# Optimization experiments

Hardware: AMD Instinct MI355X
Metric: run time of the kernel (lower is better)

Reference implementation:

```python
import jax, jax.numpy as jnp
import numpy as np

B, L = 2, 4096
EMBED_DIM, NUM_HEADS, WINDOW = 1024, 16, 256
NUM_EXPERTS, TOP_K, FF_HIDDEN = 8, 2, 4096
ENTROPY_W, MAX_USAGE = 0.1, 0.3


def setup_inputs() -> dict:
    key = jax.random.key(0)
    ks = jax.random.split(key, 10)
    s = 0.02
    C, F, E = EMBED_DIM, FF_HIDDEN, NUM_EXPERTS
    return {
        "x": jax.random.normal(ks[0], (B, L, C), jnp.float32),
        "g1": jnp.ones((C,), jnp.float32), "b1": jnp.zeros((C,), jnp.float32),
        "g2": jnp.ones((C,), jnp.float32), "b2": jnp.zeros((C,), jnp.float32),
        "g3": jnp.ones((C,), jnp.float32), "b3": jnp.zeros((C,), jnp.float32),
        "Wqkv": jax.random.normal(ks[1], (C, 3 * C), jnp.float32) * s, "bqkv": jnp.zeros((3 * C,), jnp.float32),
        "Wo": jax.random.normal(ks[2], (C, C), jnp.float32) * s, "bo": jnp.zeros((C,), jnp.float32),
        "conv_w": jax.random.normal(ks[3], (C, C, 3), jnp.float32) * s, "conv_b": jnp.zeros((C,), jnp.float32),
        "gate_W": jax.random.normal(ks[4], (C, E), jnp.float32) * s, "gate_b": jnp.zeros((E,), jnp.float32),
        "expert_W": jax.random.normal(ks[5], (E, C, C), jnp.float32) * s, "expert_b": jnp.zeros((E, C), jnp.float32),
        "ff_W1": jax.random.normal(ks[6], (C, F), jnp.float32) * s, "ff_b1": jnp.zeros((F,), jnp.float32),
        "ff_W2": jax.random.normal(ks[7], (F, C), jnp.float32) * s, "ff_b2": jnp.zeros((C,), jnp.float32),
    }


def _ln(x, g, b):
    mu = x.mean(-1, keepdims=True)
    var = ((x - mu) ** 2).mean(-1, keepdims=True)
    return (x - mu) * jax.lax.rsqrt(var + 1e-5) * g + b


def _local_attn(x, Wqkv, bqkv, Wo, bo):
    # Faithful port of the unfold-based overlapping-window attention
    Bsz, Ln, C = x.shape
    hd = C // NUM_HEADS
    pad = (-Ln) % WINDOW
    xp = jnp.pad(x, ((0, 0), (0, pad), (0, 0)))
    Lp = Ln + pad
    qkv = (xp @ Wqkv + bqkv).reshape(Bsz, Lp, 3, NUM_HEADS, hd).transpose(2, 0, 3, 1, 4)
    q, k, v = qkv[0], qkv[1], qkv[2]  # [B,H,Lp,hd]
    step = WINDOW // 2  # bidirectional=True -> overlapping windows
    nw = (Lp - WINDOW) // step + 1
    idx = (jnp.arange(nw) * step)[:, None] + jnp.arange(WINDOW)[None, :]  # [nw,w]

    def win(t):
        # torch unfold(dim=2,size=w,step) puts window on LAST axis -> [B,H,nw,hd,w]
        return jnp.swapaxes(t[:, :, idx, :], -1, -2)

    qw, kw, vw = win(q), win(k), win(v)
    # q @ k^T over the window axis (exactly what the torch code computes)
    attn = jax.nn.softmax(jnp.einsum('bhnds,bhnes->bhnde', qw, kw) * hd ** -0.5, axis=-1)
    o = jnp.einsum('bhnde,bhnes->bhnds', attn, vw)  # [B,H,nw,hd,w]
    o = o.reshape(Bsz, NUM_HEADS, nw * WINDOW, hd).transpose(0, 2, 1, 3).reshape(Bsz, nw * WINDOW, C)
    return (o @ Wo + bo)[:, :Ln]


def _dconv(x, w, b):
    # Conv1d(C,C,k=3,dilation=2,padding='same'); w is [O,I,K]
    y = jax.lax.conv_general_dilated(jnp.swapaxes(x, 1, 2), w, (1,), 'SAME',
                                     rhs_dilation=(2,), dimension_numbers=('NCH', 'OIH', 'NCH'))
    return jnp.swapaxes(y + b[None, :, None], 1, 2)


def _moe(x, gW, gb, eW, eb):
    Bsz, S, C = x.shape
    N = Bsz * S
    xf = x.reshape(N, C)
    probs = jax.nn.softmax(xf @ gW + gb, axis=-1)
    entropy = -jnp.sum(probs * jnp.log(probs + 1e-10), axis=-1).mean()
    topk_p, topk_i = jax.lax.top_k(probs, TOP_K)  # [N,K]
    # dense-equivalent top-k dispatch: out[n] = sum_k p_k * expert_{i_k}(x_n)
    eo = jnp.einsum('nc,ech->neh', xf, eW) + eb  # [N,E,C]
    combine = jnp.zeros((N, NUM_EXPERTS), xf.dtype).at[jnp.arange(N)[:, None], topk_i].add(topk_p)
    out = jnp.einsum('neh,ne->nh', eo, combine)
    counts = jnp.zeros((NUM_EXPERTS,), jnp.float32).at[topk_i.reshape(-1)].add(1.0)
    penalty = jnp.sum(jax.nn.relu(counts / N - MAX_USAGE))
    return out.reshape(Bsz, S, C), ENTROPY_W * entropy + penalty


def reference(x, g1, b1, g2, b2, g3, b3, Wqkv, bqkv, Wo, bo, conv_w, conv_b,
              gate_W, gate_b, expert_W, expert_b, ff_W1, ff_b1, ff_W2, ff_b2):
    x = x + _local_attn(_ln(x, g1, b1), Wqkv, bqkv, Wo, bo)
    x = x + _dconv(_ln(x, g2, b2), conv_w, conv_b)
    moe_out, aux = _moe(_ln(x, g3, b3), gate_W, gate_b, expert_W, expert_b)
    x = x + moe_out
    x = x + (jax.nn.gelu(x @ ff_W1 + ff_b1, approximate=False) @ ff_W2 + ff_b2)
    return x, aux
```

## Files before the change

### kernel.cpp

```cpp
#include <hip/hip_runtime.h>
#include <cmath>

typedef _Float16 f16;
typedef __attribute__((ext_vector_type(8))) _Float16 f16x8;
typedef __attribute__((ext_vector_type(4))) _Float16 f16x4;
typedef __attribute__((ext_vector_type(4))) float f32x4;

struct TileInfo { int m0, mcnt, e, pad; };

__device__ __forceinline__ void gload16(const void* g, void* l) {
  __builtin_amdgcn_global_load_lds((const __attribute__((address_space(1))) void*)g,
                                   (__attribute__((address_space(3))) void*)l, 16, 0, 0);
}

__device__ __forceinline__ float fast_gelu(float u) {
  const float c = u * (0.7978845608028654f + 0.0356774081f * u * u);
  const float t = fminf(2.0f * c, 80.0f);
  const float e = __expf(t);
  return u * (e * __builtin_amdgcn_rcpf(e + 1.0f));
}

template<int NPASS, int MODE, int EPI>
__global__ __launch_bounds__(256)
void gemm_kernel(const f16* __restrict__ Ah, const f16* __restrict__ Al, int lda,
                 const f16* __restrict__ Bh, const f16* __restrict__ Bl, int ldb,
                 const float* __restrict__ bias, const float* __restrict__ res,
                 float* __restrict__ outf, f16* __restrict__ outh, int ldo, int K,
                 const int* __restrict__ rowmap, const TileInfo* __restrict__ table,
                 const char* __restrict__ zbuf) {
  __shared__ __align__(16) char lds[65536];

  const int tid  = threadIdx.x;
  const int wave = tid >> 6;
  const int lane = tid & 63;

  int m0, mcnt, eidx = 0;
  if (MODE == 2) {
    TileInfo ti = table[blockIdx.x];
    if (ti.mcnt <= 0) return;
    m0 = ti.m0; mcnt = ti.mcnt; eidx = ti.e;
  } else { m0 = blockIdx.x * 128; mcnt = 128; }
  const int n0 = blockIdx.y * 128;

  const f16* Bh_ = Bh;
  const float* bias_ = bias;
  size_t adelta = 0, bdelta = 0;
  if (NPASS == 3) {
    adelta = (size_t)((const char*)Al - (const char*)Ah);
    bdelta = (size_t)((const char*)Bl - (const char*)Bh);
  }
  if (MODE == 2) { Bh_ += ((size_t)eidx << 20); bias_ += eidx * 1024; }

  f32x4 acc[4][4] = {};
  const int wm  = (wave >> 1) * 64;
  const int wn  = (wave & 1) * 64;
  const int fr  = lane & 15;
  const int kgb = (lane >> 4) * 16;
  const int wuni = wave * 1024;

  if constexpr (NPASS == 1) {
    const int sr    = tid / 8;
    const int cbyte = (tid % 8) * 16;
    const char* aSrc[4];
    const char* bSrc[4];
    #pragma unroll
    for (int r = 0; r < 4; ++r) {
      const int mr  = sr + r * 32;
      const int cbs = cbyte ^ ((mr & 7) << 4);
      int gi = m0 + ((mr < mcnt) ? mr : (mcnt - 1));
      if (MODE == 1 || MODE == 2) gi = rowmap[gi];
      aSrc[r] = (const char*)Ah + (size_t)gi * lda * 2 + cbs;
      const int nr   = sr + r * 32;
      const int ncbs = cbyte ^ ((nr & 7) << 4);
      bSrc[r] = (const char*)Bh_ + (size_t)(n0 + nr) * ldb * 2 + ncbs;
    }
    const int NT = K / 64;
    #pragma unroll
    for (int r = 0; r < 4; ++r) {
      gload16(aSrc[r], lds + r * 4096 + wuni);
      gload16(bSrc[r], lds + 16384 + r * 4096 + wuni);
    }
    #pragma unroll
    for (int r = 0; r < 4; ++r) {
      gload16(aSrc[r] + 128, lds + 32768 + r * 4096 + wuni);
      gload16(bSrc[r] + 128, lds + 32768 + 16384 + r * 4096 + wuni);
    }
    asm volatile("s_waitcnt vmcnt(8)" ::: "memory");
    __builtin_amdgcn_s_barrier();

    for (int kt = 0; kt < NT; ++kt) {
      const int c = kt & 1;
      const char* LAp = lds + c * 32768;
      const char* LBp = LAp + 16384;
      f16x8 ah[2][4], bh[2][4];
      #pragma unroll
      for (int kk = 0; kk < 2; ++kk) {
        #pragma unroll
        for (int i = 0; i < 4; ++i) {
          const int ar = wm + i * 16 + fr;
          ah[kk][i] = *(const f16x8*)(LAp + ar * 128 + ((kk * 64 + kgb) ^ ((ar & 7) << 4)));
          const int br = wn + i * 16 + fr;
          bh[kk][i] = *(const f16x8*)(LBp + br * 128 + ((kk * 64 + kgb) ^ ((br & 7) << 4)));
        }
      }
      asm volatile("s_waitcnt lgkmcnt(0)" ::: "memory");
      __builtin_amdgcn_s_barrier();
      if (kt + 2 < NT) {
        const size_t ko = (size_t)(kt + 2) * 128;
        #pragma unroll
        for (int r = 0; r < 4; ++r) {
          gload16(aSrc[r] + ko, lds + c * 32768 + r * 4096 + wuni);
          gload16(bSrc[r] + ko, lds + c * 32768 + 16384 + r * 4096 + wuni);
        }
      }
      #pragma unroll
      for (int kk = 0; kk < 2; ++kk)
        #pragma unroll
        for (int i = 0; i < 4; ++i)
          #pragma unroll
          for (int j = 0; j < 4; ++j)
            acc[i][j] = __builtin_amdgcn_mfma_f32_16x16x32_f16(ah[kk][i], bh[kk][j], acc[i][j], 0, 0, 0);
      if (kt + 2 < NT) asm volatile("s_waitcnt vmcnt(8)" ::: "memory");
      else             asm volatile("s_waitcnt vmcnt(0)" ::: "memory");
      __builtin_amdgcn_s_barrier();
    }
  } else {
    const int sr3 = tid >> 2;
    const int cb3 = (tid & 3) * 16;
    int aRow3[2], aCbs3[2], aOff3[2], bOff3[2];
    #pragma unroll
    for (int q = 0; q < 2; ++q) {
      const int row = q * 64 + sr3;
      const int cbs = cb3 ^ (((row >> 1) & 3) << 4);
      int gi = m0 + row;
      if (MODE == 1) gi = rowmap[m0 + row];
      aRow3[q] = gi; aCbs3[q] = cbs;
      aOff3[q] = gi * lda * 2 + cbs;
      bOff3[q] = (n0 + row) * ldb * 2 + cbs;
    }
    const int NT = K / 32;

    auto STAGE3 = [&](int kt2, char* bb) {
      const int k0 = kt2 * 32;
      #pragma unroll
      for (int q = 0; q < 2; ++q) {
        const char* as; const char* asl;
        if (MODE == 3) {
          const int tap = k0 >> 10;
          const int kc  = k0 & 1023;
          const int tok = aRow3[q] & 4095;
          const int st  = tok + (tap - 1) * 2;
          if (st >= 0 && st < 4096) {
            as  = (const char*)Ah + (size_t)(aRow3[q] + (tap - 1) * 2) * 2048 + kc * 2 + aCbs3[q];
            asl = as + adelta;
          } else { as = zbuf; asl = zbuf; }
        } else {
          as  = (const char*)Ah + (size_t)aOff3[q] + (size_t)k0 * 2;
          asl = as + adelta;
        }
        gload16(as,  bb + q * 4096 + wuni);
        gload16(asl, bb + 8192 + q * 4096 + wuni);
        const char* bs = (const char*)Bh_ + (size_t)bOff3[q] + (size_t)k0 * 2;
        gload16(bs,          bb + 16384 + q * 4096 + wuni);
        gload16(bs + bdelta, bb + 24576 + q * 4096 + wuni);
      }
    };

    STAGE3(0, lds);
    STAGE3(1, lds + 32768);
    asm volatile("s_waitcnt vmcnt(8)" ::: "memory");
    __builtin_amdgcn_s_barrier();

    for (int kt = 0; kt < NT; ++kt) {
      char* bb = lds + (kt & 1) * 32768;
      f16x8 ah[4], al[4], bh[4], bl[4];
      #pragma unroll
      for (int i = 0; i < 4; ++i) {
        const int ar = wm + i * 16 + fr;
        const int ao = ar * 64 + (kgb ^ (((ar >> 1) & 3) << 4));
        ah[i] = *(const f16x8*)(bb + ao);
        al[i] = *(const f16x8*)(bb + 8192 + ao);
        const int br = wn + i * 16 + fr;
        const int bo = br * 64 + (kgb ^ (((br >> 1) & 3) << 4));
        bh[i] = *(const f16x8*)(bb + 16384 + bo);
        bl[i] = *(const f16x8*)(bb + 24576 + bo);
      }
      asm volatile("s_waitcnt lgkmcnt(0)" ::: "memory");
      __builtin_amdgcn_s_barrier();
      if (kt + 2 < NT) STAGE3(kt + 2, bb);
      #pragma unroll
      for (int i = 0; i < 4; ++i)
        #pragma unroll
        for (int j = 0; j < 4; ++j) {
          acc[i][j] = __builtin_amdgcn_mfma_f32_16x16x32_f16(ah[i], bh[j], acc[i][j], 0, 0, 0);
          acc[i][j] = __builtin_amdgcn_mfma_f32_16x16x32_f16(ah[i], bl[j], acc[i][j], 0, 0, 0);
          acc[i][j] = __builtin_amdgcn_mfma_f32_16x16x32_f16(al[i], bh[j], acc[i][j], 0, 0, 0);
        }
      if (kt + 2 < NT) asm volatile("s_waitcnt vmcnt(8)" ::: "memory");
      else             asm volatile("s_waitcnt vmcnt(0)" ::: "memory");
      __builtin_amdgcn_s_barrier();
    }
  }

  #pragma unroll
  for (int i = 0; i < 4; ++i) {
    const int mb = wm + i * 16 + (lane >> 4) * 4;
    #pragma unroll
    for (int j = 0; j < 4; ++j) {
      const int nc = n0 + wn + j * 16 + fr;
      const float bv = bias_[nc];
      #pragma unroll
      for (int q = 0; q < 4; ++q) {
        const int ml = mb + q;
        if (MODE == 2 && ml >= mcnt) continue;
        const size_t orow = (size_t)(m0 + ml);
        float v = acc[i][j][q] + bv;
        if (EPI == 1) v += res[orow * ldo + nc];
        if (EPI == 3) v = fast_gelu(v);
        if (EPI <= 1) outf[orow * ldo + nc] = v;
        else          outh[orow * ldo + nc] = (f16)v;
      }
    }
  }
}

template<int WLO, int WGATE>
__global__ __launch_bounds__(256)
void ln_kernel(const float* __restrict__ x, const float* __restrict__ g, const float* __restrict__ b,
               f16* __restrict__ oh, f16* __restrict__ ol,
               const float* __restrict__ gW, const float* __restrict__ gb,
               float* __restrict__ logits) {
  const int row = blockIdx.x;
  const int t = threadIdx.x;
  const float4 v = ((const float4*)(x + (size_t)row * 1024))[t];
  float s  = v.x + v.y + v.z + v.w;
  float ss = v.x * v.x + v.y * v.y + v.z * v.z + v.w * v.w;
  #pragma unroll
  for (int off = 32; off; off >>= 1) { s += __shfl_down(s, off, 64); ss += __shfl_down(ss, off, 64); }
  __shared__ float red[8];
  if ((t & 63) == 0) { red[t >> 6] = s; red[(t >> 6) + 4] = ss; }
  __syncthreads();
  s  = red[0] + red[1] + red[2] + red[3];
  ss = red[4] + red[5] + red[6] + red[7];
  const float mu  = s * (1.0f / 1024.0f);
  const float var = ss * (1.0f / 1024.0f) - mu * mu;
  const float inv = 1.0f / sqrtf(var + 1e-5f);
  const float4 gv = ((const float4*)g)[t];
  const float4 bv = ((const float4*)b)[t];
  float y[4];
  y[0] = (v.x - mu) * inv * gv.x + bv.x;
  y[1] = (v.y - mu) * inv * gv.y + bv.y;
  y[2] = (v.z - mu) * inv * gv.z + bv.z;
  y[3] = (v.w - mu) * inv * gv.w + bv.w;
  f16x4 hv;
  #pragma unroll
  for (int u = 0; u < 4; ++u) hv[u] = (f16)y[u];
  *(f16x4*)(oh + (size_t)row * 1024 + t * 4) = hv;
  if (WLO) {
    f16x4 lv;
    #pragma unroll
    for (int u = 0; u < 4; ++u) lv[u] = (f16)(y[u] - (float)hv[u]);
    *(f16x4*)(ol + (size_t)row * 1024 + t * 4) = lv;
  }
  if (WGATE) {
    const float* gr = gW + (size_t)(t * 4) * 8;
    float lg[8];
    #pragma unroll
    for (int e = 0; e < 8; ++e)
      lg[e] = y[0] * gr[e] + y[1] * gr[8 + e] + y[2] * gr[16 + e] + y[3] * gr[24 + e];
    #pragma unroll
    for (int m = 1; m < 64; m <<= 1)
      #pragma unroll
      for (int e = 0; e < 8; ++e) lg[e] += __shfl_xor(lg[e], m, 64);
    __shared__ float gred[4][8];
    if ((t & 63) == 0) {
      #pragma unroll
      for (int e = 0; e < 8; ++e) gred[t >> 6][e] = lg[e];
    }
    __syncthreads();
    if (t < 8)
      logits[(size_t)row * 8 + t] = gred[0][t] + gred[1][t] + gred[2][t] + gred[3][t] + gb[t];
  }
}

__global__ __launch_bounds__(512, 4)
void attn_kernel(const float* __restrict__ qkv, f16* __restrict__ oh, f16* __restrict__ ol) {
  __shared__ __align__(16) char sm[81920];
  const int bid = blockIdx.x;
  const int b = bid >> 8, h = (bid >> 4) & 15, n = bid & 15;
  const int t = threadIdx.x;
  const size_t rowbase = (size_t)(b * 2176 + n * 128);
  const char* qg = (const char*)(qkv + rowbase * 3072 + h * 64);
  const char* kg = qg + 4096;
  const char* vg = qg + 8192;

  const int srow = t >> 4;
  const int scol = (t & 15) * 16;
  const int wuni = (t >> 6) * 1024;

  const int dt = t >> 4;
  const int et = t & 15;
  float pacc[2][4] = {};

  for (int r = 0; r < 2; ++r) {
    #pragma unroll
    for (int p = 0; p < 4; ++p) {
      const size_t off = (size_t)(r * 128 + p * 32 + srow) * 12288 + scol;
      gload16(qg + off, sm + p * 8192 + wuni);
      gload16(kg + off, sm + 32768 + p * 8192 + wuni);
    }
    __syncthreads();
    #pragma unroll 4
    for (int s = 0; s < 128; ++s) {
      const float2 q2 = *(const float2*)(sm + s * 256 + dt * 8);
      const f32x4 k4 = *(const f32x4*)(sm + 32768 + s * 256 + et * 16);
      #pragma unroll
      for (int z = 0; z < 4; ++z) {
        pacc[0][z] += q2.x * k4[z];
        pacc[1][z] += q2.y * k4[z];
      }
    }
    __syncthreads();
  }

  #pragma unroll
  for (int i = 0; i < 2; ++i) {
    #pragma unroll
    for (int z = 0; z < 4; ++z) pacc[i][z] *= 0.125f;
    float m = fmaxf(fmaxf(pacc[i][0], pacc[i][1]), fmaxf(pacc[i][2], pacc[i][3]));
    m = fmaxf(m, __shfl_xor(m, 1, 16));
    m = fmaxf(m, __shfl_xor(m, 2, 16));
    m = fmaxf(m, __shfl_xor(m, 4, 16));
    m = fmaxf(m, __shfl_xor(m, 8, 16));
    float den = 0.0f;
    #pragma unroll
    for (int z = 0; z < 4; ++z) { pacc[i][z] = __expf(pacc[i][z] - m); den += pacc[i][z]; }
    den += __shfl_xor(den, 1, 16);
    den += __shfl_xor(den, 2, 16);
    den += __shfl_xor(den, 4, 16);
    den += __shfl_xor(den, 8, 16);
    const float dinv = 1.0f / den;
    f32x4 pv;
    #pragma unroll
    for (int z = 0; z < 4; ++z) pv[z] = pacc[i][z] * dinv;
    *(f32x4*)(sm + 65536 + (dt * 2 + i) * 256 + et * 16) = pv;
  }

  const int dt2 = t & 15;
  const int st  = t >> 4;
  const int ch  = h * 64 + (st & 15) * 4;
  const size_t rb2 = (size_t)(b * 4096 + n * 256);

  for (int c = 0; c < 2; ++c) {
    __syncthreads();
    #pragma unroll
    for (int p = 0; p < 4; ++p) {
      const size_t off = (size_t)(c * 128 + p * 32 + srow) * 12288 + scol;
      gload16(vg + off, sm + p * 8192 + wuni);
    }
    __syncthreads();
    float o[16];
    #pragma unroll
    for (int u = 0; u < 16; ++u) o[u] = 0.0f;
    #pragma unroll 2
    for (int e4 = 0; e4 < 16; ++e4) {
      f32x4 p4[4], v4[4];
      #pragma unroll
      for (int i = 0; i < 4; ++i)
        p4[i] = *(const f32x4*)(sm + 65536 + (dt2 * 4 + i) * 256 + e4 * 16);
      #pragma unroll
      for (int j = 0; j < 4; ++j)
        v4[j] = *(const f32x4*)(sm + (st * 4 + j) * 256 + e4 * 16);
      #pragma unroll
      for (int j = 0; j < 4; ++j)
        #pragma unroll
        for (int i = 0; i < 4; ++i) {
          o[j * 4 + i] += v4[j][0] * p4[i][0] + v4[j][1] * p4[i][1]
                        + v4[j][2] * p4[i][2] + v4[j][3] * p4[i][3];
        }
    }
    const int rq = c * 2 + (st >> 4);
    #pragma unroll
    for (int i = 0; i < 4; ++i) {
      const size_t row = rb2 + (size_t)(dt2 * 4 + i) * 4 + rq;
      f16x4 hv, lv;
      #pragma unroll
      for (int j = 0; j < 4; ++j) {
        const float val = o[j * 4 + i];
        hv[j] = (f16)val;
        lv[j] = (f16)(val - (float)hv[j]);
      }
      *(f16x4*)(oh + row * 1024 + ch) = hv;
      *(f16x4*)(ol + row * 1024 + ch) = lv;
    }
  }
}

template<int SPLIT>
__global__ __launch_bounds__(256)
void transpose_kernel(const float* __restrict__ in, int R, int Cc,
                      f16* __restrict__ oh, f16* __restrict__ ol) {
  __shared__ float tile[32][33];
  const size_t mat = (size_t)blockIdx.z * R * Cc;
  in += mat; oh += mat; if (SPLIT) ol += mat;
  const int tx = threadIdx.x & 31, ty = threadIdx.x >> 5;
  const int c = blockIdx.x * 32 + tx;
  #pragma unroll
  for (int j = 0; j < 32; j += 8) {
    const int r = blockIdx.y * 32 + ty + j;
    tile[ty + j][tx] = in[(size_t)r * Cc + c];
  }
  __syncthreads();
  const int rT = blockIdx.y * 32 + tx;
  #pragma unroll
  for (int j = 0; j < 32; j += 8) {
    const int cT = blockIdx.x * 32 + ty + j;
    const float v = tile[tx][ty + j];
    const f16 hv = (f16)v;
    oh[(size_t)cT * R + rT] = hv;
    if (SPLIT) ol[(size_t)cT * R + rT] = (f16)(v - (float)hv);
  }
}

__global__ __launch_bounds__(256)
void convw_kernel(const float* __restrict__ w, f16* __restrict__ oh, f16* __restrict__ ol) {
  const int id = blockIdx.x * 256 + threadIdx.x;
  const int o = id >> 10, i = id & 1023;
  const float* ws = w + (size_t)o * 3072 + i * 3;
  #pragma unroll
  for (int tap = 0; tap < 3; ++tap) {
    const float v = ws[tap];
    const f16 hv = (f16)v;
    const size_t oi = (size_t)o * 3072 + tap * 1024 + i;
    oh[oi] = hv;
    ol[oi] = (f16)(v - (float)hv);
  }
}

__global__ void qkvrows_kernel(int* __restrict__ rows) {
  const int r = blockIdx.x * 256 + threadIdx.x;
  if (r < 4352) rows[r] = (r >= 2176) ? (4096 + r - 2176) : r;
}

__global__ __launch_bounds__(256)
void gatefin_kernel(const float* __restrict__ logits, float* __restrict__ top2p,
                    int* __restrict__ top2i, float* __restrict__ ent,
                    int* __restrict__ counts) {
  __shared__ int hist[8];
  const int t = threadIdx.x;
  if (t < 8) hist[t] = 0;
  __syncthreads();
  const int token = blockIdx.x * 256 + t;
  float lg[8];
  const float4 l0 = ((const float4*)(logits + (size_t)token * 8))[0];
  const float4 l1 = ((const float4*)(logits + (size_t)token * 8))[1];
  lg[0] = l0.x; lg[1] = l0.y; lg[2] = l0.z; lg[3] = l0.w;
  lg[4] = l1.x; lg[5] = l1.y; lg[6] = l1.z; lg[7] = l1.w;
  int i0 = 0; float v0 = lg[0];
  #pragma unroll
  for (int e = 1; e < 8; ++e) if (lg[e] > v0) { v0 = lg[e]; i0 = e; }
  int i1 = 0; float v1 = -1e30f;
  #pragma unroll
  for (int e = 0; e < 8; ++e) if (e != i0 && lg[e] > v1) { v1 = lg[e]; i1 = e; }
  float den = 0.0f; float pr[8];
  #pragma unroll
  for (int e = 0; e < 8; ++e) { pr[e] = __expf(lg[e] - v0); den += pr[e]; }
  const float dinv = 1.0f / den;
  float H = 0.0f, p0 = 0.0f, p1 = 0.0f;
  #pragma unroll
  for (int e = 0; e < 8; ++e) {
    const float p = pr[e] * dinv;
    H -= p * __logf(p + 1e-10f);
    if (e == i0) p0 = p;
    if (e == i1) p1 = p;
  }
  ent[token] = H;
  top2p[token * 2] = p0; top2p[token * 2 + 1] = p1;
  top2i[token * 2] = i0; top2i[token * 2 + 1] = i1;
  atomicAdd(&hist[i0], 1);
  atomicAdd(&hist[i1], 1);
  __syncthreads();
  if (t < 8) atomicAdd(&counts[t], hist[t]);
}

__global__ __launch_bounds__(256)
void scan_kernel(const float* __restrict__ ent, const int* __restrict__ counts,
                 int* __restrict__ offs, TileInfo* __restrict__ table, float* __restrict__ auxout) {
  __shared__ float red[256];
  const int t = threadIdx.x;
  float s = 0.0f;
  for (int k = 0; k < 32; ++k) s += ent[t + (k << 8)];
  red[t] = s; __syncthreads();
  for (int hh = 128; hh > 0; hh >>= 1) { if (t < hh) red[t] += red[t + hh]; __syncthreads(); }
  if (t == 0) {
    const float entmean = red[0] * (1.0f / 8192.0f);
    float pen = 0.0f; int off = 0; int nt = 0;
    for (int e = 0; e < 8; ++e) {
      const int c = counts[e];
      offs[e] = off;
      for (int m = 0; m < c; m += 128) {
        table[nt].m0 = off + m;
        table[nt].mcnt = (c - m < 128) ? (c - m) : 128;
        table[nt].e = e; table[nt].pad = 0;
        ++nt;
      }
      off += c;
      const float fr = (float)c * (1.0f / 8192.0f) - 0.3f;
      pen += (fr > 0.0f) ? fr : 0.0f;
    }
    for (; nt < 160; ++nt) { table[nt].m0 = 0; table[nt].mcnt = 0; table[nt].e = 0; table[nt].pad = 0; }
    auxout[0] = 0.1f * entmean + pen;
  }
}

__global__ __launch_bounds__(256)
void scatter_kernel(const int* __restrict__ top2i, const int* __restrict__ offs,
                    int* __restrict__ fill, int* __restrict__ moe_rows,
                    int* __restrict__ row2slot) {
  __shared__ int hist[8];
  __shared__ int base[8];
  const int t = threadIdx.x;
  if (t < 8) hist[t] = 0;
  __syncthreads();
  const int id = blockIdx.x * 256 + t;
  const int e = top2i[id];
  const int myrank = atomicAdd(&hist[e], 1);
  __syncthreads();
  if (t < 8) base[t] = atomicAdd(&fill[t], hist[t]);
  __syncthreads();
  const int row = offs[e] + base[e] + myrank;
  moe_rows[row] = id >> 1;
  row2slot[id] = row;
}

__global__ __launch_bounds__(256)
void combine_kernel(const float* __restrict__ x2, const f16* __restrict__ eo,
                    const float* __restrict__ top2p, const int* __restrict__ row2slot,
                    float* __restrict__ x3, f16* __restrict__ x3h) {
  const int n = blockIdx.x;
  const int t = threadIdx.x;
  const int r0 = row2slot[n * 2], r1 = row2slot[n * 2 + 1];
  const float p0 = top2p[n * 2], p1 = top2p[n * 2 + 1];
  const float4 xv = ((const float4*)(x2 + (size_t)n * 1024))[t];
  const f16x4 e0 = ((const f16x4*)(eo + (size_t)r0 * 1024))[t];
  const f16x4 e1 = ((const f16x4*)(eo + (size_t)r1 * 1024))[t];
  float4 o;
  o.x = xv.x + p0 * (float)e0[0] + p1 * (float)e1[0];
  o.y = xv.y + p0 * (float)e0[1] + p1 * (float)e1[1];
  o.z = xv.z + p0 * (float)e0[2] + p1 * (float)e1[2];
  o.w = xv.w + p0 * (float)e0[3] + p1 * (float)e1[3];
  ((float4*)(x3 + (size_t)n * 1024))[t] = o;
  f16x4 hv; hv[0] = (f16)o.x; hv[1] = (f16)o.y; hv[2] = (f16)o.z; hv[3] = (f16)o.w;
  ((f16x4*)(x3h + (size_t)n * 1024))[t] = hv;
}

extern "C" void kernel_launch(void* const* d_in, const int* in_sizes, int n_in,
                              void* d_out, int out_size, void* d_ws, size_t ws_size,
                              hipStream_t stream) {
  (void)in_sizes; (void)n_in; (void)out_size; (void)ws_size;
  const float* x     = (const float*)d_in[0];
  const float* g1    = (const float*)d_in[1];
  const float* b1    = (const float*)d_in[2];
  const float* g2    = (const float*)d_in[3];
  const float* b2    = (const float*)d_in[4];
  const float* g3    = (const float*)d_in[5];
  const float* b3    = (const float*)d_in[6];
  const float* Wqkv  = (const float*)d_in[7];
  const float* bqkv  = (const float*)d_in[8];
  const float* Wo    = (const float*)d_in[9];
  const float* bo    = (const float*)d_in[10];
  const float* convw = (const float*)d_in[11];
  const float* convb = (const float*)d_in[12];
  const float* gateW = (const float*)d_in[13];
  const float* gateb = (const float*)d_in[14];
  const float* expW  = (const float*)d_in[15];
  const float* expb  = (const float*)d_in[16];
  const float* ffW1  = (const float*)d_in[17];
  const float* ffb1  = (const float*)d_in[18];
  const float* ffW2  = (const float*)d_in[19];
  const float* ffb2  = (const float*)d_in[20];
  float* out = (float*)d_out;

  char* W = (char*)d_ws;
  f16* wqkvT_h = (f16*)(W + 0);
  f16* wqkvT_l = (f16*)(W + 6291456);
  f16* woT_h   = (f16*)(W + 12582912);
  f16* woT_l   = (f16*)(W + 14680064);
  f16* wcvT_h  = (f16*)(W + 16777216);
  f16* wcvT_l  = (f16*)(W + 23068672);
  f16* wexpT   = (f16*)(W + 29360128);
  f16* wff1T   = (f16*)(W + 46137344);
  f16* wff2T   = (f16*)(W + 54525952);
  char* META   = W + 62914560;
  int* counts    = (int*)(META);
  int* fill      = (int*)(META + 32);
  int* offs      = (int*)(META + 64);
  TileInfo* table = (TileInfo*)(META + 128);
  char* zbuf     = META + 3072;
  int* qkv_rows  = (int*)(META + 4096);
  float* ent     = (float*)(META + 24576);
  float* top2p   = (float*)(META + 57344);
  int* top2i     = (int*)(META + 122880);
  int* moe_rows  = (int*)(META + 188416);
  int* row2slot  = (int*)(META + 253952);
  float* logits  = (float*)(META + 327680);
  char* SA = W + 63963136;
  char* SB = W + 97517568;
  char* SC = W + 164626432;
  char* SD = W + 198180864;
  char* SE = W + 231735296;

  f16* ln1h = (f16*)SA;            f16* ln1l = (f16*)(SA + 16777216);
  f16* ln2h = ln1h;                f16* ln2l = ln1l;
  f16* ln3h = ln1h;                f16* x3h  = (f16*)(SA + 16777216);
  float* qkvbuf = (float*)SB;
  float* x2buf  = (float*)SB;
  f16*   hbuf   = (f16*)SB;
  f16* attnh = (f16*)SC;           f16* attnl = (f16*)(SC + 16777216);
  float* x1 = (float*)SD;
  f16* eobuf = (f16*)SD;
  float* x3 = (float*)SE;

  hipMemsetAsync((void*)META, 0, 4096, stream);

  dim3 blk(256);
  transpose_kernel<1><<<dim3(96, 32, 1), blk, 0, stream>>>(Wqkv, 1024, 3072, wqkvT_h, wqkvT_l);
  transpose_kernel<1><<<dim3(32, 32, 1), blk, 0, stream>>>(Wo, 1024, 1024, woT_h, woT_l);
  convw_kernel<<<4096, blk, 0, stream>>>(convw, wcvT_h, wcvT_l);
  transpose_kernel<0><<<dim3(32, 32, 8), blk, 0, stream>>>(expW, 1024, 1024, wexpT, nullptr);
  transpose_kernel<0><<<dim3(128, 32, 1), blk, 0, stream>>>(ffW1, 1024, 4096, wff1T, nullptr);
  transpose_kernel<0><<<dim3(32, 128, 1), blk, 0, stream>>>(ffW2, 4096, 1024, wff2T, nullptr);
  qkvrows_kernel<<<17, blk, 0, stream>>>(qkv_rows);

  ln_kernel<1, 0><<<8192, blk, 0, stream>>>(x, g1, b1, ln1h, ln1l, nullptr, nullptr, nullptr);
  gemm_kernel<3, 1, 0><<<dim3(34, 24), blk, 0, stream>>>(ln1h, ln1l, 1024, wqkvT_h, wqkvT_l, 1024,
      bqkv, nullptr, qkvbuf, nullptr, 3072, 1024, qkv_rows, nullptr, nullptr);
  attn_kernel<<<512, dim3(512), 0, stream>>>(qkvbuf, attnh, attnl);
  gemm_kernel<3, 0, 1><<<dim3(64, 8), blk, 0, stream>>>(attnh, attnl, 1024, woT_h, woT_l, 1024,
      bo, x, x1, nullptr, 1024, 1024, nullptr, nullptr, nullptr);
  ln_kernel<1, 0><<<8192, blk, 0, stream>>>(x1, g2, b2, ln2h, ln2l, nullptr, nullptr, nullptr);
  gemm_kernel<3, 3, 1><<<dim3(64, 8), blk, 0, stream>>>(ln2h, ln2l, 1024, wcvT_h, wcvT_l, 3072,
      convb, x1, x2buf, nullptr, 1024, 3072, nullptr, nullptr, zbuf);
  ln_kernel<0, 1><<<8192, blk, 0, stream>>>(x2buf, g3, b3, ln3h, nullptr, gateW, gateb, logits);
  gatefin_kernel<<<32, blk, 0, stream>>>(logits, top2p, top2i, ent, counts);
  scan_kernel<<<1, blk, 0, stream>>>(ent, counts, offs, table, out + 8388608);
  scatter_kernel<<<64, blk, 0, stream>>>(top2i, offs, fill, moe_rows, row2slot);
  gemm_kernel<1, 2, 2><<<dim3(136, 8), blk, 0, stream>>>(ln3h, nullptr, 1024, wexpT, nullptr, 1024,
      expb, nullptr, nullptr, eobuf, 1024, 1024, moe_rows, table, nullptr);
  combine_kernel<<<8192, blk, 0, stream>>>(x2buf, eobuf, top2p, row2slot, x3, x3h);
  gemm_kernel<1, 0, 3><<<dim3(64, 32), blk, 0, stream>>>(x3h, nullptr, 1024, wff1T, nullptr, 1024,
      ffb1, nullptr, nullptr, hbuf, 4096, 1024, nullptr, nullptr, nullptr);
  gemm_kernel<1, 0, 1><<<dim3(64, 8), blk, 0, stream>>>(hbuf, nullptr, 4096, wff2T, nullptr, 4096,
      ffb2, x3, out, nullptr, 1024, 4096, nullptr, nullptr, nullptr);
}
```

Baseline: 770.0 us.

## Use register-staged single-buffer K=64 pipeline for split-fp16 3-pass GEMM

Replaces the async global-to-LDS double-buffered K=32 pipeline in the 3-pass (hi/lo split) GEMM path with a K=64 tile. Global loads now go into registers while the current tile is computed, then are written to a single LDS buffer after a barrier. The LDS row stride and swizzle change to the 128-byte layout used by the 1-pass path. The aim is fewer barriers per K and more MFMA work per load. In exchange it uses 16 more vector registers, serializes the LDS write phase, and loses the async direct-to-LDS overlap.

```diff
diff --git a/kernel.cpp b/kernel.cpp
--- a/kernel.cpp
+++ b/kernel.cpp
@@ -58,9 +58,10 @@
   const int kgb = (lane >> 4) * 16;
   const int wuni = wave * 1024;
 
+  const int sr    = tid / 8;
+  const int cbyte = (tid % 8) * 16;
+
   if constexpr (NPASS == 1) {
-    const int sr    = tid / 8;
-    const int cbyte = (tid % 8) * 16;
     const char* aSrc[4];
     const char* bSrc[4];
     #pragma unroll
@@ -70,9 +71,7 @@
       int gi = m0 + ((mr < mcnt) ? mr : (mcnt - 1));
       if (MODE == 1 || MODE == 2) gi = rowmap[gi];
       aSrc[r] = (const char*)Ah + (size_t)gi * lda * 2 + cbs;
-      const int nr   = sr + r * 32;
-      const int ncbs = cbyte ^ ((nr & 7) << 4);
-      bSrc[r] = (const char*)Bh_ + (size_t)(n0 + nr) * ldb * 2 + ncbs;
+      bSrc[r] = (const char*)Bh_ + (size_t)(n0 + mr) * ldb * 2 + cbs;
     }
     const int NT = K / 64;
     #pragma unroll
@@ -125,79 +124,91 @@
       __builtin_amdgcn_s_barrier();
     }
   } else {
-    const int sr3 = tid >> 2;
-    const int cb3 = (tid & 3) * 16;
-    int aRow3[2], aCbs3[2], aOff3[2], bOff3[2];
-    #pragma unroll
-    for (int q = 0; q < 2; ++q) {
-      const int row = q * 64 + sr3;
-      const int cbs = cb3 ^ (((row >> 1) & 3) << 4);
-      int gi = m0 + row;
-      if (MODE == 1) gi = rowmap[m0 + row];
-      aRow3[q] = gi; aCbs3[q] = cbs;
-      aOff3[q] = gi * lda * 2 + cbs;
-      bOff3[q] = (n0 + row) * ldb * 2 + cbs;
-    }
-    const int NT = K / 32;
-
-    auto STAGE3 = [&](int kt2, char* bb) {
-      const int k0 = kt2 * 32;
-      #pragma unroll
-      for (int q = 0; q < 2; ++q) {
+    const char* aSrcB[4]; const char* bSrcB[4];
+    int aRowC[4], aCbs[4];
+    #pragma unroll
+    for (int r = 0; r < 4; ++r) {
+      const int mr  = sr + r * 32;
+      const int cbs = cbyte ^ ((mr & 7) << 4);
+      int gi = m0 + mr;
+      if (MODE == 1) gi = rowmap[gi];
+      if (MODE == 3) { aRowC[r] = gi; aCbs[r] = cbs; aSrcB[r] = nullptr; }
+      else           { aSrcB[r] = (const char*)Ah + (size_t)gi * lda * 2 + cbs; aRowC[r] = 0; aCbs[r] = 0; }
+      bSrcB[r] = (const char*)Bh_ + (size_t)(n0 + mr) * ldb * 2 + cbs;
+    }
+    const int NT = K / 64;
+    f32x4 st[16];
+
+    auto SLOAD = [&](int k0) {
+      #pragma unroll
+      for (int r = 0; r < 4; ++r) {
         const char* as; const char* asl;
         if (MODE == 3) {
           const int tap = k0 >> 10;
           const int kc  = k0 & 1023;
-          const int tok = aRow3[q] & 4095;
-          const int st  = tok + (tap - 1) * 2;
-          if (st >= 0 && st < 4096) {
-            as  = (const char*)Ah + (size_t)(aRow3[q] + (tap - 1) * 2) * 2048 + kc * 2 + aCbs3[q];
+          const int tok = aRowC[r] & 4095;
+          const int stk = tok + (tap - 1) * 2;
+          if (stk >= 0 && stk < 4096) {
+            as  = (const char*)Ah + (size_t)(aRowC[r] + (tap - 1) * 2) * 2048 + kc * 2 + aCbs[r];
             asl = as + adelta;
           } else { as = zbuf; asl = zbuf; }
         } else {
-          as  = (const char*)Ah + (size_t)aOff3[q] + (size_t)k0 * 2;
+          as  = aSrcB[r] + (size_t)k0 * 2;
           asl = as + adelta;
         }
-        gload16(as,  bb + q * 4096 + wuni);
-        gload16(asl, bb + 8192 + q * 4096 + wuni);
-        const char* bs = (const char*)Bh_ + (size_t)bOff3[q] + (size_t)k0 * 2;
-        gload16(bs,          bb + 16384 + q * 4096 + wuni);
-        gload16(bs + bdelta, bb + 24576 + q * 4096 + wuni);
+        st[r * 4 + 0] = *(const f32x4*)as;
+        st[r * 4 + 1] = *(const f32x4*)asl;
+        const char* bs = bSrcB[r] + (size_t)k0 * 2;
+        st[r * 4 + 2] = *(const f32x4*)bs;
+        st[r * 4 + 3] = *(const f32x4*)(bs + bdelta);
       }
     };
-
-    STAGE3(0, lds);
-    STAGE3(1, lds + 32768);
-    asm volatile("s_waitcnt vmcnt(8)" ::: "memory");
-    __builtin_amdgcn_s_barrier();
+    auto SWRITE = [&]() {
+      #pragma unroll
+      for (int r = 0; r < 4; ++r) {
+        *(f32x4*)(lds + 0     + r * 4096 + tid * 16) = st[r * 4 + 0];
+        *(f32x4*)(lds + 16384 + r * 4096 + tid * 16) = st[r * 4 + 1];
+        *(f32x4*)(lds + 32768 + r * 4096 + tid * 16) = st[r * 4 + 2];
+        *(f32x4*)(lds + 49152 + r * 4096 + tid * 16) = st[r * 4 + 3];
+      }
+    };
+
+    SLOAD(0);
+    SWRITE();
+    __syncthreads();
 
     for (int kt = 0; kt < NT; ++kt) {
-      char* bb = lds + (kt & 1) * 32768;
-      f16x8 ah[4], al[4], bh[4], bl[4];
-      #pragma unroll
-      for (int i = 0; i < 4; ++i) {
-        const int ar = wm + i * 16 + fr;
-        const int ao = ar * 64 + (kgb ^ (((ar >> 1) & 3) << 4));
-        ah[i] = *(const f16x8*)(bb + ao);
-        al[i] = *(const f16x8*)(bb + 8192 + ao);
-        const int br = wn + i * 16 + fr;
-        const int bo = br * 64 + (kgb ^ (((br >> 1) & 3) << 4));
-        bh[i] = *(const f16x8*)(bb + 16384 + bo);
-        bl[i] = *(const f16x8*)(bb + 24576 + bo);
+      if (kt + 1 < NT) SLOAD((kt + 1) * 64);
+      #pragma unroll
+      for (int kk = 0; kk < 2; ++kk) {
+        f16x8 ah[4], al[4], bh[4], bl[4];
+        #pragma unroll
+        for (int i = 0; i < 4; ++i) {
+          const int ar = wm + i * 16 + fr;
+          const int ao = ar * 128 + ((kk * 64 + kgb) ^ ((ar & 7) << 4));
+          ah[i] = *(const f16x8*)(lds + ao);
+          al[i] = *(const f16x8*)(lds + 16384 + ao);
+          const int br = wn + i * 16 + fr;
+          const int bo = br * 128 + ((kk * 64 + kgb) ^ ((br & 7) << 4));
+          bh[i] = *(const f16x8*)(lds + 32768 + bo);
+          bl[i] = *(const f16x8*)(lds + 49152 + bo);
+        }
+        #pragma unroll
+        for (int i = 0; i < 4; ++i) {
+          #pragma unroll
+          for (int j = 0; j < 4; ++j) {
+            acc[i][j] = __builtin_amdgcn_mfma_f32_16x16x32_f16(ah[i], bh[j], acc[i][j], 0, 0, 0);
+            acc[i][j] = __builtin_amdgcn_mfma_f32_16x16x32_f16(ah[i], bl[j], acc[i][j], 0, 0, 0);
+            acc[i][j] = __builtin_amdgcn_mfma_f32_16x16x32_f16(al[i], bh[j], acc[i][j], 0, 0, 0);
+          }
+        }
       }
       asm volatile("s_waitcnt lgkmcnt(0)" ::: "memory");
       __builtin_amdgcn_s_barrier();
-      if (kt + 2 < NT) STAGE3(kt + 2, bb);
-      #pragma unroll
-      for (int i = 0; i < 4; ++i)
-        #pragma unroll
-        for (int j = 0; j < 4; ++j) {
-          acc[i][j] = __builtin_amdgcn_mfma_f32_16x16x32_f16(ah[i], bh[j], acc[i][j], 0, 0, 0);
-          acc[i][j] = __builtin_amdgcn_mfma_f32_16x16x32_f16(ah[i], bl[j], acc[i][j], 0, 0, 0);
-          acc[i][j] = __builtin_amdgcn_mfma_f32_16x16x32_f16(al[i], bh[j], acc[i][j], 0, 0, 0);
-        }
-      if (kt + 2 < NT) asm volatile("s_waitcnt vmcnt(8)" ::: "memory");
-      else             asm volatile("s_waitcnt vmcnt(0)" ::: "memory");
+      if (kt + 1 < NT) {
+        SWRITE();
+        asm volatile("s_waitcnt lgkmcnt(0)" ::: "memory");
+      }
       __builtin_amdgcn_s_barrier();
     }
   }
```

New measurement: 765.3 us. Within noise of the previous version (-0.6%).
